# Kernel optimization log

Hardware: AMD Instinct MI355X
Metric: run time of the kernel (lower is better)

Reference implementation:

```python
import jax, jax.numpy as jnp
import numpy as np

jax.config.update("jax_enable_x64", True)

P = 2038074743          # prime used by the ROBE-Z hash
BLOCK_K = 32            # tile sizes of the hashed reconstruction (kernel tile)
BLOCK_N = 32
INPUT_DIM = 8192
OUTPUT_DIM = 8192
HASH_SIZE = 1 << 22     # compressed parameter count
TOKENS = 512


def setup_inputs() -> dict:
    key = jax.random.key(0)
    k1, k2 = jax.random.split(key, 2)
    x = jax.random.normal(k1, (TOKENS, INPUT_DIM), dtype=jnp.float32)
    hashed_weight = jax.random.normal(k2, (HASH_SIZE,), dtype=jnp.float32) * 0.02
    bias = jnp.zeros((OUTPUT_DIM,), dtype=jnp.float32)
    # mirrors RzLinear._generate_random_numbers(seed): 4 random ints made even, prepended with P
    rng = np.random.RandomState(1024)
    r = rng.randint(0, P, size=(4,)).astype(np.int64)
    r = r + (r % 2)
    random_numbers = jnp.asarray(np.concatenate([np.array([P], dtype=np.int64), r]), dtype=jnp.int64)
    return {"x": x, "hashed_weight": hashed_weight, "bias": bias, "random_numbers": random_numbers}


def _weight_indices(random_numbers):
    """Hashed flat indices into hashed_weight for the dense [K, N] weight."""
    K, N = INPUT_DIM, OUTPUT_DIM
    kt, nt = K // BLOCK_K, N // BLOCK_N
    R1, R2, R3 = random_numbers[1], random_numbers[2], random_numbers[3]
    k_ids = jnp.arange(kt, dtype=jnp.int64)
    n_ids = jnp.arange(nt, dtype=jnp.int64)
    # per-tile start offset into the compressed array
    start = ((k_ids[:, None] * R3 + n_ids[None, :] * R2 + R1) % P) % (HASH_SIZE - BLOCK_K * BLOCK_N + 1)
    start = start.astype(jnp.int32)  # [kt, nt]
    off = (jnp.arange(BLOCK_K, dtype=jnp.int32)[:, None] * BLOCK_N
           + jnp.arange(BLOCK_N, dtype=jnp.int32)[None, :])  # [BK, BN], row-major within tile
    idx = start[:, None, :, None] + off[None, :, None, :]    # [kt, BK, nt, BN]
    return idx.reshape(K, N)


def reference(x, hashed_weight, bias, random_numbers):
    idx = _weight_indices(random_numbers)          # [K, N] int32
    W = hashed_weight[idx]                          # hashed-gather reconstruction, [K, N]
    out = jnp.matmul(x, W) + bias[None, :]          # [tokens, N]
    return out
```

## Files before the change

### kernel.cpp

```cpp
#include <hip/hip_runtime.h>
#include <hip/hip_fp16.h>

#define NDIM 8192
#define KDIM 8192
#define NT 256
#define MOD2 4193281
#define PRIME 2038074743LL

#define BM 256
#define BN 128
#define BK 32
#define KITER 64
#define BSLAB 1032

typedef _Float16 half8 __attribute__((ext_vector_type(8)));
typedef float floatx4 __attribute__((ext_vector_type(4)));

__global__ __launch_bounds__(256) void prep_kernel(const float* __restrict__ x,
                                                   const float* __restrict__ hw,
                                                   const float* __restrict__ bias,
                                                   const int* __restrict__ rn,
                                                   __half* __restrict__ xh,
                                                   __half* __restrict__ hh,
                                                   int* __restrict__ starts,
                                                   float* __restrict__ out) {
    int b = blockIdx.x;
    int tid = threadIdx.x;
    if (b < 8192) {
        int i = b * 256 + tid;
        const float4* s; __half2* d; int j;
        if (i < (1 << 20)) { s = (const float4*)x;  d = (__half2*)xh; j = i; }
        else               { s = (const float4*)hw; d = (__half2*)hh; j = i - (1 << 20); }
        float4 v = s[j];
        d[j * 2]     = __floats2half2_rn(v.x, v.y);
        d[j * 2 + 1] = __floats2half2_rn(v.z, v.w);
    } else if (b < 8192 + 4096) {
        int i = (b - 8192) * 256 + tid;
        float4 bv = *(const float4*)(bias + ((i & 2047) << 2));
        ((float4*)out)[i] = bv;
    } else {
        int t = (b - 12288) * 256 + tid;
        bool is64 = (rn[1] == 0 && rn[3] == 0);
        long long R1 = is64 ? rn[2] : rn[1];
        long long R2 = is64 ? rn[4] : rn[2];
        long long R3 = is64 ? rn[6] : rn[3];
        long long k_id = t >> 8, n_id = t & 255;
        long long v = (k_id * R3 + n_id * R2 + R1) % PRIME;
        starts[t] = (int)(v % MOD2);
    }
}

__device__ __forceinline__ void gload16(const __half* g, __half* l) {
    __builtin_amdgcn_global_load_lds((const __attribute__((address_space(1))) void*)g,
                                     (__attribute__((address_space(3))) void*)l, 16, 0, 0);
}

__global__ __launch_bounds__(512, 4) void gemm_kernel(
    const __half* __restrict__ xh, const __half* __restrict__ hh,
    const int* __restrict__ starts, float* __restrict__ out) {
    __shared__ __align__(16) __half As[2][BM * 32];
    __shared__ __align__(16) __half Bs[2][4 * BSLAB];
    __shared__ int Ss[KITER * 4];

    const int tid = threadIdx.x;
    const int lane = tid & 63;
    const int wave = tid >> 6;
    const int wm = wave >> 1;
    const int wn = wave & 1;
    const int quad = lane >> 4;
    const int l16 = lane & 15;

    const int i = blockIdx.x;
    const int ks = i & 3;
    const int m_blk = (i >> 2) & 1;
    const int n_blk = i >> 3;
    const int gm0 = m_blk * BM;
    const int gn0 = n_blk * BN;
    const int kt0 = ks * KITER;
    const int n_id0 = n_blk * 4;

    if (tid < KITER * 4) {
        int kp = tid >> 2, tile = tid & 3;
        Ss[tid] = starts[(kt0 + kp) * NT + n_id0 + tile];
    }

    const int a_t = wave * 2;
    const int a_chunk = (lane & 3) ^ ((lane >> 3) & 3);
    const __half* a_g0 = xh + (size_t)(gm0 + a_t * 16 + (lane >> 2)) * KDIM
                         + kt0 * 32 + a_chunk * 8;
    const __half* a_g1 = a_g0 + (size_t)16 * KDIM;

#define STAGE_A(buf_, kp_) do {                                                \
        gload16(a_g0 + (kp_) * 32, &As[buf_][a_t * 512]);                      \
        gload16(a_g1 + (kp_) * 32, &As[buf_][a_t * 512 + 512]);                \
    } while (0)

    const int b_tile = tid >> 7;
    const int t7 = tid & 127;
    const int b_np = t7 & 15;
    const int b_kg = t7 >> 4;
    const int b_oct = b_kg >> 1;
    const unsigned b_base = b_oct * BSLAB;
    const unsigned b_pos = (b_tile * 32 + 2 * b_np) * 8 + (b_kg & 1) * 4;
    const unsigned bswz = (b_np & 4) << 1;

    unsigned pbA0, pbA1, pbA2, pbA3, pbB0, pbB1, pbB2, pbB3;

#define LOADT(Q0, Q1, Q2, Q3, kp_) do {                                        \
        int st = Ss[(kp_) * 4 + b_tile];                                       \
        const __half* src = hh + st + b_kg * 128 + b_np * 2;                   \
        Q0 = *(const unsigned*)(src);                                          \
        Q1 = *(const unsigned*)(src + 32);                                     \
        Q2 = *(const unsigned*)(src + 64);                                     \
        Q3 = *(const unsigned*)(src + 96);                                     \
    } while (0)

#define STORET(Q0, Q1, Q2, Q3, buf_) do {                                      \
        unsigned lo0 = (Q0 & 0xffffu) | (Q1 << 16);                            \
        unsigned lo1 = (Q2 & 0xffffu) | (Q3 << 16);                            \
        unsigned hi0 = (Q0 >> 16) | (Q1 & 0xffff0000u);                        \
        unsigned hi1 = (Q2 >> 16) | (Q3 & 0xffff0000u);                        \
        uint2 e = {lo0, lo1}, o = {hi0, hi1};                                  \
        *(uint2*)&Bs[buf_][b_base + (b_pos ^ bswz)] = e;                       \
        *(uint2*)&Bs[buf_][b_base + ((b_pos + 8) ^ bswz)] = o;                 \
    } while (0)

    floatx4 acc[4][4];
#pragma unroll
    for (int r = 0; r < 4; r++)
#pragma unroll
        for (int c = 0; c < 4; c++)
            acc[r][c] = (floatx4){0.f, 0.f, 0.f, 0.f};

    const unsigned rswz = (unsigned)(l16 & 8);
    const unsigned a_rswz = (unsigned)((l16 >> 1) & 3);

#define FRAGS_MFMA(buf_) do {                                                  \
        half8 af[4], bf[4];                                                    \
        _Pragma("unroll")                                                      \
        for (int r = 0; r < 4; r++)                                            \
            af[r] = *(const half8*)&As[buf_][(unsigned)(wm * 64 + r * 16 + l16) * 32 \
                                             + ((quad ^ a_rswz) * 8)];         \
        _Pragma("unroll")                                                      \
        for (int c = 0; c < 4; c++)                                            \
            bf[c] = *(const half8*)&Bs[buf_][quad * BSLAB + ((unsigned)((wn * 64 + c * 16 + l16) * 8) ^ rswz)]; \
        _Pragma("unroll")                                                      \
        for (int r = 0; r < 4; r++)                                            \
            _Pragma("unroll")                                                  \
            for (int c = 0; c < 4; c++)                                        \
                acc[r][c] = __builtin_amdgcn_mfma_f32_16x16x32_f16(af[r], bf[c], acc[r][c], 0, 0, 0); \
    } while (0)

    __syncthreads();
    STAGE_A(0, 0);
    LOADT(pbA0, pbA1, pbA2, pbA3, 0);
    LOADT(pbB0, pbB1, pbB2, pbB3, 1);
    STORET(pbA0, pbA1, pbA2, pbA3, 0);
    __syncthreads();

    for (int kp = 0; kp < KITER; kp += 2) {
        STAGE_A(1, kp + 1);
        if (kp + 2 < KITER) LOADT(pbA0, pbA1, pbA2, pbA3, kp + 2);
        FRAGS_MFMA(0);
        STORET(pbB0, pbB1, pbB2, pbB3, 1);
        __syncthreads();

        if (kp + 2 < KITER) STAGE_A(0, kp + 2);
        if (kp + 3 < KITER) LOADT(pbB0, pbB1, pbB2, pbB3, kp + 3);
        FRAGS_MFMA(1);
        if (kp + 2 < KITER)
            STORET(pbA0, pbA1, pbA2, pbA3, 0);
        __syncthreads();
    }

#pragma unroll
    for (int c = 0; c < 4; c++) {
        int col = gn0 + wn * 64 + c * 16 + l16;
#pragma unroll
        for (int r = 0; r < 4; r++) {
            int row0 = gm0 + wm * 64 + r * 16 + quad * 4;
#pragma unroll
            for (int e = 0; e < 4; e++)
                atomicAdd(&out[(size_t)(row0 + e) * NDIM + col], acc[r][c][e]);
        }
    }
#undef LOADT
#undef STORET
#undef FRAGS_MFMA
#undef STAGE_A
}

extern "C" void kernel_launch(void* const* d_in, const int* in_sizes, int n_in,
                              void* d_out, int out_size, void* d_ws, size_t ws_size,
                              hipStream_t stream) {
    const float* x = (const float*)d_in[0];
    const float* hw = (const float*)d_in[1];
    const float* bias = (const float*)d_in[2];
    const int* rn = (const int*)d_in[3];
    float* out = (float*)d_out;

    char* ws = (char*)d_ws;
    __half* xh = (__half*)ws;
    __half* hh = (__half*)(ws + (8u << 20));
    int* starts = (int*)(ws + (16u << 20));

    hipLaunchKernelGGL(prep_kernel, dim3(12544), dim3(256), 0, stream,
                       x, hw, bias, rn, xh, hh, starts, out);
    hipLaunchKernelGGL(gemm_kernel, dim3(512), dim3(512), 0, stream, xh, hh, starts, out);
}
```

Measured before the change: 198.4 us.

## Hand-schedule GEMM main loop with explicit waitcnt, barriers and MFMA priority

```diff
diff --git a/kernel.cpp b/kernel.cpp
--- a/kernel.cpp
+++ b/kernel.cpp
@@ -55,6 +55,8 @@
                                      (__attribute__((address_space(3))) void*)l, 16, 0, 0);
 }
 
+#define SBAR() __builtin_amdgcn_sched_barrier(0)
+
 __global__ __launch_bounds__(512, 4) void gemm_kernel(
     const __half* __restrict__ xh, const __half* __restrict__ hh,
     const int* __restrict__ starts, float* __restrict__ out) {
@@ -135,20 +137,38 @@
     const unsigned rswz = (unsigned)(l16 & 8);
     const unsigned a_rswz = (unsigned)((l16 >> 1) & 3);
 
-#define FRAGS_MFMA(buf_) do {                                                  \
-        half8 af[4], bf[4];                                                    \
-        _Pragma("unroll")                                                      \
-        for (int r = 0; r < 4; r++)                                            \
-            af[r] = *(const half8*)&As[buf_][(unsigned)(wm * 64 + r * 16 + l16) * 32 \
-                                             + ((quad ^ a_rswz) * 8)];         \
-        _Pragma("unroll")                                                      \
-        for (int c = 0; c < 4; c++)                                            \
-            bf[c] = *(const half8*)&Bs[buf_][quad * BSLAB + ((unsigned)((wn * 64 + c * 16 + l16) * 8) ^ rswz)]; \
-        _Pragma("unroll")                                                      \
-        for (int r = 0; r < 4; r++)                                            \
-            _Pragma("unroll")                                                  \
-            for (int c = 0; c < 4; c++)                                        \
-                acc[r][c] = __builtin_amdgcn_mfma_f32_16x16x32_f16(af[r], bf[c], acc[r][c], 0, 0, 0); \
+    half8 fa0, fa1, fa2, fa3, fb0, fb1, fb2, fb3;
+
+#define READF(buf_) do {                                                       \
+        fa0 = *(const half8*)&As[buf_][(unsigned)(wm * 64 +  0 + l16) * 32 + ((quad ^ a_rswz) * 8)]; \
+        fa1 = *(const half8*)&As[buf_][(unsigned)(wm * 64 + 16 + l16) * 32 + ((quad ^ a_rswz) * 8)]; \
+        fa2 = *(const half8*)&As[buf_][(unsigned)(wm * 64 + 32 + l16) * 32 + ((quad ^ a_rswz) * 8)]; \
+        fa3 = *(const half8*)&As[buf_][(unsigned)(wm * 64 + 48 + l16) * 32 + ((quad ^ a_rswz) * 8)]; \
+        fb0 = *(const half8*)&Bs[buf_][quad * BSLAB + ((unsigned)((wn * 64 +  0 + l16) * 8) ^ rswz)]; \
+        fb1 = *(const half8*)&Bs[buf_][quad * BSLAB + ((unsigned)((wn * 64 + 16 + l16) * 8) ^ rswz)]; \
+        fb2 = *(const half8*)&Bs[buf_][quad * BSLAB + ((unsigned)((wn * 64 + 32 + l16) * 8) ^ rswz)]; \
+        fb3 = *(const half8*)&Bs[buf_][quad * BSLAB + ((unsigned)((wn * 64 + 48 + l16) * 8) ^ rswz)]; \
+    } while (0)
+
+#define MFMAC() do {                                                           \
+        __builtin_amdgcn_s_setprio(1);                                         \
+        acc[0][0] = __builtin_amdgcn_mfma_f32_16x16x32_f16(fa0, fb0, acc[0][0], 0, 0, 0); \
+        acc[1][0] = __builtin_amdgcn_mfma_f32_16x16x32_f16(fa1, fb0, acc[1][0], 0, 0, 0); \
+        acc[2][0] = __builtin_amdgcn_mfma_f32_16x16x32_f16(fa2, fb0, acc[2][0], 0, 0, 0); \
+        acc[3][0] = __builtin_amdgcn_mfma_f32_16x16x32_f16(fa3, fb0, acc[3][0], 0, 0, 0); \
+        acc[0][1] = __builtin_amdgcn_mfma_f32_16x16x32_f16(fa0, fb1, acc[0][1], 0, 0, 0); \
+        acc[1][1] = __builtin_amdgcn_mfma_f32_16x16x32_f16(fa1, fb1, acc[1][1], 0, 0, 0); \
+        acc[2][1] = __builtin_amdgcn_mfma_f32_16x16x32_f16(fa2, fb1, acc[2][1], 0, 0, 0); \
+        acc[3][1] = __builtin_amdgcn_mfma_f32_16x16x32_f16(fa3, fb1, acc[3][1], 0, 0, 0); \
+        acc[0][2] = __builtin_amdgcn_mfma_f32_16x16x32_f16(fa0, fb2, acc[0][2], 0, 0, 0); \
+        acc[1][2] = __builtin_amdgcn_mfma_f32_16x16x32_f16(fa1, fb2, acc[1][2], 0, 0, 0); \
+        acc[2][2] = __builtin_amdgcn_mfma_f32_16x16x32_f16(fa2, fb2, acc[2][2], 0, 0, 0); \
+        acc[3][2] = __builtin_amdgcn_mfma_f32_16x16x32_f16(fa3, fb2, acc[3][2], 0, 0, 0); \
+        acc[0][3] = __builtin_amdgcn_mfma_f32_16x16x32_f16(fa0, fb3, acc[0][3], 0, 0, 0); \
+        acc[1][3] = __builtin_amdgcn_mfma_f32_16x16x32_f16(fa1, fb3, acc[1][3], 0, 0, 0); \
+        acc[2][3] = __builtin_amdgcn_mfma_f32_16x16x32_f16(fa2, fb3, acc[2][3], 0, 0, 0); \
+        acc[3][3] = __builtin_amdgcn_mfma_f32_16x16x32_f16(fa3, fb3, acc[3][3], 0, 0, 0); \
+        __builtin_amdgcn_s_setprio(0);                                         \
     } while (0)
 
     __syncthreads();
@@ -159,18 +179,35 @@
     __syncthreads();
 
     for (int kp = 0; kp < KITER; kp += 2) {
+        READF(0);
         STAGE_A(1, kp + 1);
         if (kp + 2 < KITER) LOADT(pbA0, pbA1, pbA2, pbA3, kp + 2);
-        FRAGS_MFMA(0);
+        SBAR();
+        __builtin_amdgcn_s_barrier();
+        SBAR();
+        MFMAC();
         STORET(pbB0, pbB1, pbB2, pbB3, 1);
-        __syncthreads();
-
+        SBAR();
+        if (kp + 2 < KITER)
+            __builtin_amdgcn_s_waitcnt(0x0074);
+        else
+            __builtin_amdgcn_s_waitcnt(0x0070);
+        __builtin_amdgcn_s_barrier();
+        SBAR();
+
+        READF(1);
         if (kp + 2 < KITER) STAGE_A(0, kp + 2);
         if (kp + 3 < KITER) LOADT(pbB0, pbB1, pbB2, pbB3, kp + 3);
-        FRAGS_MFMA(1);
+        SBAR();
+        __builtin_amdgcn_s_barrier();
+        SBAR();
+        MFMAC();
         if (kp + 2 < KITER)
             STORET(pbA0, pbA1, pbA2, pbA3, 0);
-        __syncthreads();
+        SBAR();
+        __builtin_amdgcn_s_waitcnt(0x0074);
+        __builtin_amdgcn_s_barrier();
+        SBAR();
     }
 
 #pragma unroll
@@ -186,7 +223,8 @@
     }
 #undef LOADT
 #undef STORET
-#undef FRAGS_MFMA
+#undef READF
+#undef MFMAC
 #undef STAGE_A
 }
 
```

Measured after the change: 192.2 us. 1.03x faster.
